# Kernel optimization log

Measured on AMD Instinct MI355X. Metric: run time of the kernel, lower is better.

Reference implementation:

```python
import jax, jax.numpy as jnp
import numpy as np

P0 = 2   # tublet_size
P = 16   # patch_size
FC = 2   # flow channels (map_x, map_y)


def patchify(x, p0, p1, p2):
    # x: (B, C, T, H, W) -> (B, (T/p0)(H/p1)(W/p2), p0*p1*p2*C)
    B, C, T, H, W = x.shape
    x = x.reshape(B, C, T // p0, p0, H // p1, p1, W // p2, p2)
    x = x.transpose(0, 2, 4, 6, 3, 5, 7, 1)  # b t h w p0 p1 p2 c
    return x.reshape(B, (T // p0) * (H // p1) * (W // p2), p0 * p1 * p2 * C)


def unpatchify(x, p0, p1, p2, C, T, H, W):
    # x: (B, N, p0*p1*p2*C) -> (B, C, T, H, W)
    B = x.shape[0]
    x = x.reshape(B, T // p0, H // p1, W // p2, p0, p1, p2, C)
    x = x.transpose(0, 7, 1, 4, 2, 5, 3, 6)  # b c t p0 h p1 w p2
    return x.reshape(B, C, T, H, W)


def bilinear_warp(imgs, mx, my):
    # imgs: (B, C, T, H, W); mx, my: (B, T, H, W) absolute sample coords.
    # Equivalent of cv2.remap INTER_LINEAR with constant (zero) border.
    B, C, T, H, W = imgs.shape
    x0 = jnp.floor(mx)
    y0 = jnp.floor(my)
    wx = (mx - x0).reshape(B, 1, T, H * W)
    wy = (my - y0).reshape(B, 1, T, H * W)
    x0i = x0.astype(jnp.int32)
    y0i = y0.astype(jnp.int32)
    imgs_flat = imgs.reshape(B, C, T, H * W)

    def gather(yi, xi):
        yc = jnp.clip(yi, 0, H - 1)
        xc = jnp.clip(xi, 0, W - 1)
        idx = (yc * W + xc).reshape(B, 1, T, H * W)
        v = jnp.take_along_axis(imgs_flat, jnp.broadcast_to(idx, (B, C, T, H * W)), axis=-1)
        valid = ((yi >= 0) & (yi <= H - 1) & (xi >= 0) & (xi <= W - 1)).reshape(B, 1, T, H * W)
        return v * valid.astype(v.dtype)

    v00 = gather(y0i, x0i)
    v01 = gather(y0i, x0i + 1)
    v10 = gather(y0i + 1, x0i)
    v11 = gather(y0i + 1, x0i + 1)
    out = (v00 * (1 - wx) * (1 - wy) + v01 * wx * (1 - wy)
           + v10 * (1 - wx) * wy + v11 * wx * wy)
    return out.reshape(B, C, T, H, W)


def setup_inputs() -> dict:
    key = jax.random.key(0)
    k1, k2, k3 = jax.random.split(key, 3)
    B, C, T, H, W = 8, 3, 16, 224, 224
    N = (T // P0) * (H // P) * (W // P)         # 1568 tokens
    D = P0 * P * P * FC                         # 1024 per-token flow dim
    output = jax.random.normal(k1, (B, N, D), dtype=jnp.float32)
    raw_target = jax.random.normal(k2, (B, C, T, H, W), dtype=jnp.float32)
    mask = jax.random.randint(k3, (B, N), 0, 2) > 0
    return {"output": output, "raw_target": raw_target, "mask": mask}


def reference(output, raw_target, mask):
    B, C, T, H, W = raw_target.shape
    # tokens -> dense flow field (B, 2, T, H, W)
    flows = unpatchify(output, P0, P, P, FC, T, H, W)
    gx = jnp.arange(W, dtype=flows.dtype)               # (W,)
    gy = jnp.arange(H, dtype=flows.dtype)[:, None]      # (H, 1)
    mx = flows[:, 0] + gx                                # (B, T, H, W)
    my = flows[:, 1] + gy
    recons = bilinear_warp(raw_target, mx, my)           # (B, C, T, H, W)
    rec_p = patchify(recons, P0, P, P)                   # (B, N, p0*p1*p2*C)
    tgt_p = patchify(raw_target, P0, P, P)
    m = mask.astype(rec_p.dtype)[..., None]              # (B, N, 1)
    diff2 = (rec_p - tgt_p) ** 2 * m
    denom = jnp.maximum(m.sum(), 1.0) * rec_p.shape[-1]
    return diff2.sum() / denom
```

## Files before the change

### kernel.cpp

```cpp
#include <hip/hip_runtime.h>

#define Bd 8
#define Cd 3
#define Td 16
#define Hd 224
#define Wd 224
#define Nd 1568
#define HWd (Hd*Wd)
#define NPH 14
#define NPW 14
#define NT2 8
#define NSTRIP (Bd*NT2*NPH)
#define GRID_MAIN (NSTRIP*2)
#define HALO 2
#define SROWS (16 + 2*HALO)
#define LROW Wd
#define LPLANE (SROWS*LROW)
#define LDS_FLOATS (Cd*LPLANE)
#define STG_GRAN (Cd*SROWS*56)
#define PATCH_ELEMS 1536.0

typedef const float __attribute__((address_space(1))) gfloat;
typedef float __attribute__((address_space(3))) sfloat;

__global__ __launch_bounds__(256)
void flow_mse_strip(const float* __restrict__ outp,
                    const float* __restrict__ raw,
                    const int* __restrict__ mask,
                    float* __restrict__ partial,
                    int* __restrict__ scnt) {
    __shared__ float lds[LDS_FLOATS];
    __shared__ float sred[4];

    const int tid   = threadIdx.x;
    const int bid   = blockIdx.x;
    const int strip = bid >> 1;
    const int i0    = bid & 1;
    const int b     = strip / (NT2 * NPH);
    const int sr    = strip - b * (NT2 * NPH);
    const int t2    = sr / NPH;
    const int ph    = sr - t2 * NPH;
    const int t     = (t2 << 1) | i0;
    const int ybase = (ph << 4) - HALO;

    const float* fbase = raw + ((size_t)b * Cd * Td + t) * HWd;
    #pragma unroll
    for (int it = 0; it < 14; ++it) {
        int v = tid + (it << 8);
        if (v < STG_GRAN) {
            int c    = v / 1120;
            int rem  = v - c * 1120;
            int j    = rem / 56;
            int col4 = rem - j * 56;
            int yc   = min(max(ybase + j, 0), Hd - 1);
            const float* g = fbase + (size_t)c * (Td * HWd) + yc * Wd + (col4 << 2);
            __builtin_amdgcn_global_load_lds((gfloat*)g, (sfloat*)(lds + (v << 2)),
                                             16, 0, 0);
        }
    }

    const int nbase = t2 * 196 + ph * NPW;
    const int lane  = tid & 63;
    bool mm = false;
    if (lane < NPW) mm = (mask[b * Nd + nbase + lane] != 0);
    const unsigned mw0   = (unsigned)(__ballot(mm) & 0x3FFFull);
    const int      tkcnt = __popc(mw0);

    __syncthreads();

    float acc = 0.f;
    const int py = tid >> 4, px = tid & 15;
    const int h  = (ph << 4) + py;

    unsigned mw = mw0;
    if (mw) {
        int pw = __ffs((int)mw) - 1;
        const float* fpf = outp + (((size_t)(b * Nd + nbase + pw)) << 10) + (i0 << 9);
        float2 f = ((const float2*)fpf)[tid];

        while (1) {
            unsigned nmw = mw & (mw - 1);
            int npw = 0;
            float2 nf = make_float2(0.f, 0.f);
            if (nmw) {
                npw = __ffs((int)nmw) - 1;
                const float* nfp = outp + (((size_t)(b * Nd + nbase + npw)) << 10) + (i0 << 9);
                nf = ((const float2*)nfp)[tid];
            }

            {
                const int w = (pw << 4) + px;
                float mx = f.x + (float)w;
                float my = f.y + (float)h;
                float x0 = floorf(mx), y0 = floorf(my);
                float wx = mx - x0,    wy = my - y0;
                int x0i = (int)x0, y0i = (int)y0;
                int x1i = x0i + 1,  y1i = y0i + 1;

                bool vx0 = (x0i >= 0) && (x0i < Wd);
                bool vx1 = (x1i >= 0) && (x1i < Wd);
                bool vy0 = (y0i >= 0) && (y0i < Hd);
                bool vy1 = (y1i >= 0) && (y1i < Hd);

                float W00 = (1.f - wx) * (1.f - wy) * ((vx0 && vy0) ? 1.f : 0.f);
                float W01 = wx         * (1.f - wy) * ((vx1 && vy0) ? 1.f : 0.f);
                float W10 = (1.f - wx) * wy         * ((vx0 && vy1) ? 1.f : 0.f);
                float W11 = wx         * wy         * ((vx1 && vy1) ? 1.f : 0.f);

                int xc0 = min(max(x0i, 0), Wd - 1);
                int xc1 = min(max(x1i, 0), Wd - 1);
                int yc0 = min(max(y0i, 0), Hd - 1);
                int yc1 = min(max(y1i, 0), Hd - 1);
                int ly0 = yc0 - ybase, ly1 = yc1 - ybase;
                const int bt = (py + HALO) * LROW + w;

                if ((ly0 >= 0) & (ly1 < SROWS)) {
                    const int b00 = ly0 * LROW + xc0;
                    const int b01 = ly0 * LROW + xc1;
                    const int b10 = ly1 * LROW + xc0;
                    const int b11 = ly1 * LROW + xc1;
                    #pragma unroll
                    for (int c = 0; c < Cd; ++c) {
                        const float* pl = lds + c * LPLANE;
                        float rec = pl[b00] * W00 + pl[b01] * W01
                                  + pl[b10] * W10 + pl[b11] * W11;
                        float d = rec - pl[bt];
                        acc += d * d;
                    }
                } else {
                    const int i00 = yc0 * Wd + xc0;
                    const int i01 = yc0 * Wd + xc1;
                    const int i10 = yc1 * Wd + xc0;
                    const int i11 = yc1 * Wd + xc1;
                    #pragma unroll
                    for (int c = 0; c < Cd; ++c) {
                        const float* img = fbase + (size_t)c * (Td * HWd);
                        float rec = img[i00] * W00 + img[i01] * W01
                                  + img[i10] * W10 + img[i11] * W11;
                        float d = rec - (lds + c * LPLANE)[bt];
                        acc += d * d;
                    }
                }
            }

            if (!nmw) break;
            mw = nmw; pw = npw; f = nf;
        }
    }

    for (int off = 32; off > 0; off >>= 1) acc += __shfl_down(acc, off, 64);
    if ((tid & 63) == 0) sred[tid >> 6] = acc;
    __syncthreads();
    if (tid == 0) {
        partial[bid] = sred[0] + sred[1] + sred[2] + sred[3];
        if (i0 == 0) scnt[strip] = tkcnt;
    }
}

__global__ void finalize_kernel(const float* __restrict__ partial,
                                const int* __restrict__ scnt,
                                float* __restrict__ out) {
    const int tid = threadIdx.x;
    double s = 0.0;
    for (int i = tid; i < GRID_MAIN; i += 256) s += (double)partial[i];
    int c = 0;
    for (int i = tid; i < NSTRIP; i += 256) c += scnt[i];
    for (int off = 32; off > 0; off >>= 1) {
        s += __shfl_down(s, off, 64);
        c += __shfl_down(c, off, 64);
    }
    __shared__ double sd[4];
    __shared__ int    sc[4];
    int lane = tid & 63, wid = tid >> 6;
    if (lane == 0) { sd[wid] = s; sc[wid] = c; }
    __syncthreads();
    if (tid == 0) {
        double st = sd[0] + sd[1] + sd[2] + sd[3];
        int    ct = sc[0] + sc[1] + sc[2] + sc[3];
        double denom = (double)(ct > 0 ? ct : 1) * PATCH_ELEMS;
        out[0] = (float)(st / denom);
    }
}

extern "C" void kernel_launch(void* const* d_in, const int* in_sizes, int n_in,
                              void* d_out, int out_size, void* d_ws, size_t ws_size,
                              hipStream_t stream) {
    const float* outp = (const float*)d_in[0];
    const float* raw  = (const float*)d_in[1];
    const int*   mask = (const int*)d_in[2];
    float* out = (float*)d_out;

    float* partial = (float*)d_ws;
    int*   scnt    = (int*)((char*)d_ws + GRID_MAIN * 4);

    flow_mse_strip<<<GRID_MAIN, 256, 0, stream>>>(outp, raw, mask, partial, scnt);
    finalize_kernel<<<1, 256, 0, stream>>>(partial, scnt, out);
}
```

Baseline: 165.1 us.

## Split work per colour channel across blocks with XCD-aware mapping

Each block now handles a single colour channel of a strip instead of all three. This triples the grid and cuts the LDS footprint to a third, which is meant to raise occupancy (launch bounds now request 8 blocks per CU) and shorten each block's staging phase. Block ids are remapped so that consecutive units land on the same XCD, and the software prefetch of the next token's flow is removed. The trade-off is that each flow vector and mask word is loaded three times and the bilinear coordinate maths is repeated per channel.

```diff
diff --git a/kernel.cpp b/kernel.cpp
--- a/kernel.cpp
+++ b/kernel.cpp
@@ -11,19 +11,20 @@
 #define NPW 14
 #define NT2 8
 #define NSTRIP (Bd*NT2*NPH)
-#define GRID_MAIN (NSTRIP*2)
+#define NUNIT (NSTRIP*2)
+#define GRID_MAIN (NUNIT*3)
+#define UPX (NUNIT/8)
 #define HALO 2
 #define SROWS (16 + 2*HALO)
 #define LROW Wd
-#define LPLANE (SROWS*LROW)
-#define LDS_FLOATS (Cd*LPLANE)
-#define STG_GRAN (Cd*SROWS*56)
+#define LDS_FLOATS (SROWS*LROW)
+#define STG_GRAN (SROWS*56)
 #define PATCH_ELEMS 1536.0
 
 typedef const float __attribute__((address_space(1))) gfloat;
 typedef float __attribute__((address_space(3))) sfloat;
 
-__global__ __launch_bounds__(256)
+__global__ __launch_bounds__(256, 8)
 void flow_mse_strip(const float* __restrict__ outp,
                     const float* __restrict__ raw,
                     const int* __restrict__ mask,
@@ -32,10 +33,15 @@
     __shared__ float lds[LDS_FLOATS];
     __shared__ float sred[4];
 
-    const int tid   = threadIdx.x;
-    const int bid   = blockIdx.x;
-    const int strip = bid >> 1;
-    const int i0    = bid & 1;
+    const int tid  = threadIdx.x;
+    const int bid  = blockIdx.x;
+    const int xcd  = bid & 7;
+    const int slot = bid >> 3;
+    const int c    = slot % 3;
+    const int ul   = slot / 3;
+    const int u    = xcd * UPX + ul;
+    const int strip = u >> 1;
+    const int i0    = u & 1;
     const int b     = strip / (NT2 * NPH);
     const int sr    = strip - b * (NT2 * NPH);
     const int t2    = sr / NPH;
@@ -43,17 +49,15 @@
     const int t     = (t2 << 1) | i0;
     const int ybase = (ph << 4) - HALO;
 
-    const float* fbase = raw + ((size_t)b * Cd * Td + t) * HWd;
+    const float* plane = raw + ((size_t)(b * Cd + c) * Td + t) * HWd;
     #pragma unroll
-    for (int it = 0; it < 14; ++it) {
+    for (int it = 0; it < 5; ++it) {
         int v = tid + (it << 8);
         if (v < STG_GRAN) {
-            int c    = v / 1120;
-            int rem  = v - c * 1120;
-            int j    = rem / 56;
-            int col4 = rem - j * 56;
+            int j    = v / 56;
+            int col4 = v - j * 56;
             int yc   = min(max(ybase + j, 0), Hd - 1);
-            const float* g = fbase + (size_t)c * (Td * HWd) + yc * Wd + (col4 << 2);
+            const float* g = plane + yc * Wd + (col4 << 2);
             __builtin_amdgcn_global_load_lds((gfloat*)g, (sfloat*)(lds + (v << 2)),
                                              16, 0, 0);
         }
@@ -71,81 +75,51 @@
     float acc = 0.f;
     const int py = tid >> 4, px = tid & 15;
     const int h  = (ph << 4) + py;
+    const int bt = (py + HALO) * LROW;
 
     unsigned mw = mw0;
-    if (mw) {
-        int pw = __ffs((int)mw) - 1;
+    while (mw) {
+        const int pw = __ffs((int)mw) - 1;
+        mw &= mw - 1;
+
         const float* fpf = outp + (((size_t)(b * Nd + nbase + pw)) << 10) + (i0 << 9);
         float2 f = ((const float2*)fpf)[tid];
 
-        while (1) {
-            unsigned nmw = mw & (mw - 1);
-            int npw = 0;
-            float2 nf = make_float2(0.f, 0.f);
-            if (nmw) {
-                npw = __ffs((int)nmw) - 1;
-                const float* nfp = outp + (((size_t)(b * Nd + nbase + npw)) << 10) + (i0 << 9);
-                nf = ((const float2*)nfp)[tid];
-            }
+        const int w = (pw << 4) + px;
+        float mx = f.x + (float)w;
+        float my = f.y + (float)h;
+        float x0 = floorf(mx), y0 = floorf(my);
+        float wx = mx - x0,    wy = my - y0;
+        int x0i = (int)x0, y0i = (int)y0;
+        int x1i = x0i + 1,  y1i = y0i + 1;
 
-            {
-                const int w = (pw << 4) + px;
-                float mx = f.x + (float)w;
-                float my = f.y + (float)h;
-                float x0 = floorf(mx), y0 = floorf(my);
-                float wx = mx - x0,    wy = my - y0;
-                int x0i = (int)x0, y0i = (int)y0;
-                int x1i = x0i + 1,  y1i = y0i + 1;
+        bool vx0 = (x0i >= 0) && (x0i < Wd);
+        bool vx1 = (x1i >= 0) && (x1i < Wd);
+        bool vy0 = (y0i >= 0) && (y0i < Hd);
+        bool vy1 = (y1i >= 0) && (y1i < Hd);
 
-                bool vx0 = (x0i >= 0) && (x0i < Wd);
-                bool vx1 = (x1i >= 0) && (x1i < Wd);
-                bool vy0 = (y0i >= 0) && (y0i < Hd);
-                bool vy1 = (y1i >= 0) && (y1i < Hd);
+        float W00 = (1.f - wx) * (1.f - wy) * ((vx0 && vy0) ? 1.f : 0.f);
+        float W01 = wx         * (1.f - wy) * ((vx1 && vy0) ? 1.f : 0.f);
+        float W10 = (1.f - wx) * wy         * ((vx0 && vy1) ? 1.f : 0.f);
+        float W11 = wx         * wy         * ((vx1 && vy1) ? 1.f : 0.f);
 
-                float W00 = (1.f - wx) * (1.f - wy) * ((vx0 && vy0) ? 1.f : 0.f);
-                float W01 = wx         * (1.f - wy) * ((vx1 && vy0) ? 1.f : 0.f);
-                float W10 = (1.f - wx) * wy         * ((vx0 && vy1) ? 1.f : 0.f);
-                float W11 = wx         * wy         * ((vx1 && vy1) ? 1.f : 0.f);
+        int xc0 = min(max(x0i, 0), Wd - 1);
+        int xc1 = min(max(x1i, 0), Wd - 1);
+        int yc0 = min(max(y0i, 0), Hd - 1);
+        int yc1 = min(max(y1i, 0), Hd - 1);
+        int ly0 = yc0 - ybase, ly1 = yc1 - ybase;
 
-                int xc0 = min(max(x0i, 0), Wd - 1);
-                int xc1 = min(max(x1i, 0), Wd - 1);
-                int yc0 = min(max(y0i, 0), Hd - 1);
-                int yc1 = min(max(y1i, 0), Hd - 1);
-                int ly0 = yc0 - ybase, ly1 = yc1 - ybase;
-                const int bt = (py + HALO) * LROW + w;
-
-                if ((ly0 >= 0) & (ly1 < SROWS)) {
-                    const int b00 = ly0 * LROW + xc0;
-                    const int b01 = ly0 * LROW + xc1;
-                    const int b10 = ly1 * LROW + xc0;
-                    const int b11 = ly1 * LROW + xc1;
-                    #pragma unroll
-                    for (int c = 0; c < Cd; ++c) {
-                        const float* pl = lds + c * LPLANE;
-                        float rec = pl[b00] * W00 + pl[b01] * W01
-                                  + pl[b10] * W10 + pl[b11] * W11;
-                        float d = rec - pl[bt];
-                        acc += d * d;
-                    }
-                } else {
-                    const int i00 = yc0 * Wd + xc0;
-                    const int i01 = yc0 * Wd + xc1;
-                    const int i10 = yc1 * Wd + xc0;
-                    const int i11 = yc1 * Wd + xc1;
-                    #pragma unroll
-                    for (int c = 0; c < Cd; ++c) {
-                        const float* img = fbase + (size_t)c * (Td * HWd);
-                        float rec = img[i00] * W00 + img[i01] * W01
-                                  + img[i10] * W10 + img[i11] * W11;
-                        float d = rec - (lds + c * LPLANE)[bt];
-                        acc += d * d;
-                    }
-                }
-            }
-
-            if (!nmw) break;
-            mw = nmw; pw = npw; f = nf;
+        float tg = lds[bt + w];
+        float rec;
+        if ((ly0 >= 0) & (ly1 < SROWS)) {
+            rec = lds[ly0 * LROW + xc0] * W00 + lds[ly0 * LROW + xc1] * W01
+                + lds[ly1 * LROW + xc0] * W10 + lds[ly1 * LROW + xc1] * W11;
+        } else {
+            rec = plane[yc0 * Wd + xc0] * W00 + plane[yc0 * Wd + xc1] * W01
+                + plane[yc1 * Wd + xc0] * W10 + plane[yc1 * Wd + xc1] * W11;
         }
+        float d = rec - tg;
+        acc += d * d;
     }
 
     for (int off = 32; off > 0; off >>= 1) acc += __shfl_down(acc, off, 64);
@@ -153,7 +127,7 @@
     __syncthreads();
     if (tid == 0) {
         partial[bid] = sred[0] + sred[1] + sred[2] + sred[3];
-        if (i0 == 0) scnt[strip] = tkcnt;
+        if (c == 0 && i0 == 0) scnt[strip] = tkcnt;
     }
 }
 
```

After: 160.3 us. 2.9% less time.
